# Kernel tuning notes

Measured on AMD Instinct MI355X. Metric: run time of the kernel, lower is better.

The kernel has to match this reference:

```python
import jax, jax.numpy as jnp
import numpy as np

N = 13627
E = 504378
D = 500


def _seg_softmax(e, seg, n):
    m = jax.ops.segment_max(e, seg, num_segments=n)
    ex = jnp.exp(e - m[seg])
    s = jax.ops.segment_sum(ex, seg, num_segments=n)
    return ex / (s[seg] + 1e-16)


def _gatv2(x, src, dst, Wl, Wr, att, b, n):
    # PyG GATv2Conv (heads=1): message = Wl x_src; score uses Wl x_src + Wr x_dst
    xl = x @ Wl                                   # [N, F]
    xr = x @ Wr                                   # [N, F]
    e = jax.nn.leaky_relu(xl[src] + xr[dst], 0.2) @ att   # [E]
    a = _seg_softmax(e, dst, n)                   # segment softmax over targets
    out = jax.ops.segment_sum(a[:, None] * xl[src], dst, num_segments=n)
    return out + b


def setup_inputs() -> dict:
    key = jax.random.key(0)
    ks = jax.random.split(key, 24)
    s = 0.05
    inp = {
        'x': jax.random.normal(ks[0], (N, D), dtype=jnp.float32),
        'edge_index': jax.random.randint(ks[1], (2, E), 0, N),
        'neg_edge_index': jax.random.randint(ks[2], (2, E), 0, N),
        'Wl1': jax.random.normal(ks[3], (D, 300)) * s,
        'Wr1': jax.random.normal(ks[4], (D, 300)) * s,
        'att1': jax.random.normal(ks[5], (300,)) * s,
        'b1': jnp.zeros((300,)),
        'Wl2': jax.random.normal(ks[6], (300, 100)) * s,
        'Wr2': jax.random.normal(ks[7], (300, 100)) * s,
        'att2': jax.random.normal(ks[8], (100,)) * s,
        'b2': jnp.zeros((100,)),
        'Wl3': jax.random.normal(ks[9], (100, 1)) * s,
        'Wr3': jax.random.normal(ks[10], (100, 1)) * s,
        'att3': jax.random.normal(ks[11], (1,)) * s,
        'b3': jnp.zeros((1,)),
        'W_lin1': jax.random.normal(ks[12], (D, 100)) * s,
        'b_lin1': jnp.zeros((100,)),
        'W_lin2': jax.random.normal(ks[13], (D, 100)) * s,
        'b_lin2': jnp.zeros((100,)),
        'c1': jnp.array([0.5], dtype=jnp.float32),
        'c2': jnp.array([0.5], dtype=jnp.float32),
    }
    return inp


def reference(x, edge_index, neg_edge_index, Wl1, Wr1, att1, b1, Wl2, Wr2, att2, b2,
              Wl3, Wr3, att3, b3, W_lin1, b_lin1, W_lin2, b_lin2, c1, c2):
    # eval mode: dropout / dropout_adj are identity
    loops = jnp.arange(N)
    src = jnp.concatenate([edge_index[0], loops])   # GATv2Conv adds self loops
    dst = jnp.concatenate([edge_index[1], loops])

    h1 = jax.nn.relu(_gatv2(x, src, dst, Wl1, Wr1, att1, b1, N))
    h2 = jax.nn.relu(_gatv2(h1, src, dst, Wl2, Wr2, att2, b2, N))

    xo = h2 + jax.nn.relu(x @ W_lin1 + b_lin1)
    z = h2 + jax.nn.relu(x @ W_lin2 + b_lin2)

    # link-prediction reconstruction loss
    pos_s = jnp.sum(z[edge_index[0]] * z[edge_index[1]], axis=1)
    pos_loss = -jnp.mean(jnp.log(jax.nn.sigmoid(pos_s) + 1e-15))
    neg_s = jnp.sum(z[neg_edge_index[0]] * z[neg_edge_index[1]], axis=1)
    neg_loss = -jnp.mean(jnp.log(1.0 - jax.nn.sigmoid(neg_s) + 1e-15))
    r_loss = pos_loss + neg_loss

    out = _gatv2(xo, src, dst, Wl3, Wr3, att3, b3, N)   # [N, 1]
    return out, r_loss, c1, c2
```

## Files before the change

kernel.cpp:

```cpp
#include <hip/hip_runtime.h>
#include <hip/hip_bf16.h>

#define NODES 13627
#define DIM   500

typedef short short8 __attribute__((ext_vector_type(8)));
typedef float f32x4 __attribute__((ext_vector_type(4)));
typedef float floatx2 __attribute__((ext_vector_type(2)));

__device__ inline float wave_reduce_sum(float v) {
#pragma unroll
    for (int o = 32; o > 0; o >>= 1) v += __shfl_xor(v, o, 64);
    return v;
}

__device__ inline void store_v(float* p, float v) { *p = v; }
__device__ inline void store_v(__hip_bfloat16* p, float v) { *p = __float2bfloat16(v); }

__device__ inline float blo(unsigned w) { unsigned t = w << 16;        return __builtin_bit_cast(float, t); }
__device__ inline float bhi(unsigned w) { unsigned t = w & 0xffff0000u; return __builtin_bit_cast(float, t); }

__device__ inline unsigned char to_fp8(float v) {
    int r = __builtin_amdgcn_cvt_pk_fp8_f32(v, v, 0, false);
    return (unsigned char)(r & 0xff);
}

__device__ inline unsigned pk2bf(float a, float b) {
    unsigned la = (unsigned)__builtin_bit_cast(unsigned short, __float2bfloat16(a));
    unsigned hb = (unsigned)__builtin_bit_cast(unsigned short, __float2bfloat16(b));
    return la | (hb << 16);
}

struct b4 { __hip_bfloat16 a, b, c, d; };

__global__ __launch_bounds__(256) void hist_kernel(const int* __restrict__ dst,
                                                   int* __restrict__ cnt, int E) {
    int i = blockIdx.x * blockDim.x + threadIdx.x;
    if (i < E) atomicAdd(&cnt[dst[i]], 1);
}

__global__ __launch_bounds__(1024) void scan_kernel(int* __restrict__ cnt_cur,
                                                    int* __restrict__ off, int n) {
    __shared__ int wsum[16];
    const int tid = threadIdx.x, lane = tid & 63, w = tid >> 6;
    int carry = 0;
    for (int base = 0; base < n; base += 1024) {
        int i = base + tid;
        int v = (i < n) ? cnt_cur[i] : 0;
        int s = v;
#pragma unroll
        for (int o = 1; o < 64; o <<= 1) {
            int t = __shfl_up(s, o, 64);
            if (lane >= o) s += t;
        }
        if (lane == 63) wsum[w] = s;
        __syncthreads();
        if (w == 0 && lane < 16) {
            int x = wsum[lane];
            int sx = x;
#pragma unroll
            for (int o = 1; o < 16; o <<= 1) {
                int t = __shfl_up(sx, o, 64);
                if (lane >= o) sx += t;
            }
            wsum[lane] = sx;
        }
        __syncthreads();
        int wo = (w == 0) ? 0 : wsum[w - 1];
        int total = wsum[15];
        int excl = carry + wo + (s - v);
        if (i < n) { off[i] = excl; cnt_cur[i] = excl; }
        carry += total;
        __syncthreads();
    }
    if (tid == 0) off[n] = carry;
}

__global__ __launch_bounds__(256) void scatter_kernel(const int* __restrict__ src,
                                                      const int* __restrict__ dst,
                                                      int* __restrict__ cur,
                                                      int* __restrict__ ssrc, int E) {
    int i = blockIdx.x * blockDim.x + threadIdx.x;
    if (i < E) {
        int p = atomicAdd(&cur[dst[i]], 1);
        ssrc[p] = src[i];
    }
}

__global__ __launch_bounds__(256) void convert_all_kernel(
    const float* __restrict__ x,
    const float* __restrict__ Wl1, const float* __restrict__ Wr1,
    const float* __restrict__ Wl2, const float* __restrict__ Wr2,
    const float* __restrict__ Ws1, const float* __restrict__ Ws2,
    const float* __restrict__ bs1, const float* __restrict__ bs2,
    __hip_bfloat16* __restrict__ W1T, __hip_bfloat16* __restrict__ W2T,
    __hip_bfloat16* __restrict__ WsT, float* __restrict__ bcat,
    __hip_bfloat16* __restrict__ xb, int M) {
    int i = blockIdx.x * 256 + threadIdx.x;
    if (i < 327680) {
        int n = i >> 9, k = i & 511;
        float v = 0.f;
        if (k < 500) {
            if (n < 300) v = Wl1[k * 300 + n];
            else if (n < 600) v = Wr1[k * 300 + n - 300];
        }
        W1T[i] = __float2bfloat16(v);
    } else if (i < 409600) {
        int j = i - 327680;
        int n = j / 320, k = j - n * 320;
        float v = 0.f;
        if (k < 300) {
            if (n < 100) v = Wl2[k * 100 + n];
            else if (n < 200) v = Wr2[k * 100 + n - 100];
        }
        W2T[j] = __float2bfloat16(v);
    } else if (i < 540672) {
        int j = i - 409600;
        int n = j >> 9, k = j & 511;
        float v = 0.f;
        if (k < 500) {
            if (n < 100) v = Ws1[k * 100 + n];
            else if (n < 200) v = Ws2[k * 100 + n - 100];
        }
        WsT[j] = __float2bfloat16(v);
    } else if (i < 540928) {
        int n = i - 540672;
        float v = 0.f;
        if (n < 100) v = bs1[n];
        else if (n < 200) v = bs2[n - 100];
        bcat[n] = v;
    } else {
        int j = i - 540928;
        if (j >= M * 128) return;
        int m = j >> 7, k = (j & 127) << 2;
        b4 o;
        if (k < 500) {
            float4 v = *(const float4*)(x + (size_t)m * 500 + k);
            o.a = __float2bfloat16(v.x); o.b = __float2bfloat16(v.y);
            o.c = __float2bfloat16(v.z); o.d = __float2bfloat16(v.w);
        } else {
            o.a = o.b = o.c = o.d = __float2bfloat16(0.f);
        }
        *(b4*)(xb + (size_t)m * 512 + k) = o;
    }
}

template <int EPI, typename TC>
__global__ __launch_bounds__(256) void mfma_gemm(
    const __hip_bfloat16* __restrict__ A, const __hip_bfloat16* __restrict__ BT,
    TC* __restrict__ C, const float* __restrict__ bias, const float* __restrict__ h2,
    unsigned char* __restrict__ p8, __hip_bfloat16* __restrict__ pb,
    int M, int Kp, int Nn, int ldc) {
    __shared__ short AsF[8 * 64 * 8];
    __shared__ short BsF[4 * 64 * 8];
    const int t = threadIdx.x;
    const int w = t >> 6, lane = t & 63;
    const int c = t & 3, rr = t >> 2;
    const int m0 = blockIdx.y * 128, n0 = blockIdx.x * 64;

    f32x4 acc[2][4];
#pragma unroll
    for (int i = 0; i < 2; i++)
#pragma unroll
        for (int j = 0; j < 4; j++) acc[i][j] = (f32x4){0.f, 0.f, 0.f, 0.f};

    for (int k0 = 0; k0 < Kp; k0 += 32) {
#pragma unroll
        for (int r = 0; r < 2; r++) {
            int m = r * 64 + rr;
            int gm = m0 + m; if (gm >= M) gm = M - 1;
            float4 v = *(const float4*)(A + (size_t)gm * Kp + k0 + c * 8);
            int mi = m >> 4, sl = m & 15;
            *(float4*)(&AsF[(mi * 64 + c * 16 + sl) * 8]) = v;
        }
        {
            int n = rr;
            float4 v = *(const float4*)(BT + (size_t)(n0 + n) * Kp + k0 + c * 8);
            int ni = n >> 4, sl = n & 15;
            *(float4*)(&BsF[(ni * 64 + c * 16 + sl) * 8]) = v;
        }
        __syncthreads();
        short8 a0 = *(const short8*)(&AsF[((w * 2 + 0) * 64 + lane) * 8]);
        short8 a1 = *(const short8*)(&AsF[((w * 2 + 1) * 64 + lane) * 8]);
#pragma unroll
        for (int j = 0; j < 4; j++) {
            short8 b = *(const short8*)(&BsF[(j * 64 + lane) * 8]);
            acc[0][j] = __builtin_amdgcn_mfma_f32_16x16x32_bf16(a0, b, acc[0][j], 0, 0, 0);
            acc[1][j] = __builtin_amdgcn_mfma_f32_16x16x32_bf16(a1, b, acc[1][j], 0, 0, 0);
        }
        __syncthreads();
    }

    const int q = lane >> 4, sl = lane & 15;
#pragma unroll
    for (int i = 0; i < 2; i++) {
#pragma unroll
        for (int j = 0; j < 4; j++) {
#pragma unroll
            for (int reg = 0; reg < 4; reg++) {
                int gm = m0 + w * 32 + i * 16 + q * 4 + reg;
                int gn = n0 + j * 16 + sl;
                if (gm >= M) continue;
                float v = acc[i][j][reg];
                if constexpr (EPI == 1) {
                    if (gn < 300)       p8[(size_t)gm * 304 + gn] = to_fp8(v);
                    else if (gn < 600)  pb[(size_t)gm * 320 + (gn - 300)] = __float2bfloat16(v);
                    else if (gn < 620)  pb[(size_t)gm * 320 + (gn - 300)] = __float2bfloat16(0.f);
                    else if (gn < 624)  p8[(size_t)gm * 304 + (gn - 320)] = 0;
                } else if constexpr (EPI == 2) {
                    if (gn < 100)       p8[(size_t)gm * 112 + gn] = to_fp8(v);
                    else if (gn < 200)  pb[(size_t)gm * 128 + (gn - 100)] = __float2bfloat16(v);
                    else if (gn < 212)  p8[(size_t)gm * 112 + (gn - 100)] = 0;
                    else if (gn < 240)  pb[(size_t)gm * 128 + (gn - 112)] = __float2bfloat16(0.f);
                } else if constexpr (EPI == 3) {
                    if (gn < 200) {
                        int cn = gn < 100 ? gn : gn - 100;
                        float val = fmaxf(v + bias[gn], 0.f) + h2[(size_t)gm * 100 + cn];
                        if (gn < 100) C[(size_t)gm * 100 + gn] = val;
                        else p8[(size_t)gm * 128 + (gn - 100)] = to_fp8(val);
                    } else if (gn < 228) {
                        p8[(size_t)gm * 128 + (gn - 100)] = 0;
                    }
                } else {
                    store_v(&C[(size_t)gm * ldc + gn], v);
                }
            }
        }
    }
}

template <int F, int NJ, int SL8, int SRB, int SOUT, int JSL, typename TOUT>
__global__ __launch_bounds__(256) void gat_f8_kernel(
    const unsigned char* __restrict__ xl8, const __hip_bfloat16* __restrict__ xrb,
    const float* __restrict__ att, const float* __restrict__ bias,
    const int* __restrict__ off, const int* __restrict__ ssrc,
    TOUT* __restrict__ out, int n) {
    __shared__ float sden[2];
    __shared__ float sacc[2][NJ * 64];
    const int t = threadIdx.x;
    const int lane = t & 63;
    const int sl = lane & 15, q = lane >> 4;
    const int half = (t >> 6) & 1;
    const int pairIdx = t >> 7;
    int wid = blockIdx.x * 2 + pairIdx;
    if (wid >= n) wid = n - 1;

    floatx2 attv[NJ * 2], xrv[NJ * 2], acc[NJ * 2];
    const unsigned* xru = (const unsigned*)xrb + (size_t)wid * (SRB / 2);
#pragma unroll
    for (int j = 0; j < NJ; j++) {
        const int f0 = sl * 4 + j * 64;
        if (f0 < F) {
            float4 a4 = *(const float4*)(att + f0);
            attv[j * 2 + 0] = (floatx2){a4.x, a4.y};
            attv[j * 2 + 1] = (floatx2){a4.z, a4.w};
        } else {
            attv[j * 2 + 0] = (floatx2){0.f, 0.f};
            attv[j * 2 + 1] = (floatx2){0.f, 0.f};
        }
        unsigned u0 = __builtin_nontemporal_load(xru + (f0 >> 1));
        unsigned u1 = __builtin_nontemporal_load(xru + (f0 >> 1) + 1);
        xrv[j * 2 + 0] = (floatx2){blo(u0), bhi(u0)};
        xrv[j * 2 + 1] = (floatx2){blo(u1), bhi(u1)};
        acc[j * 2 + 0] = (floatx2){0.f, 0.f};
        acc[j * 2 + 1] = (floatx2){0.f, 0.f};
    }

    const int s0 = off[wid], s1 = off[wid + 1];
    const int h0 = (s1 - s0) >> 1;
    const int eb = half ? (s0 + h0) : (s0 - 1);
    const int ee = half ? s1 : (s0 + h0);
    float den = 0.f;

    unsigned u[NJ];
    {
        int eq = eb + q;
        int src = wid;
        if (eq >= s0 && eq < ee) src = __builtin_nontemporal_load(ssrc + eq);
        const unsigned char* row = xl8 + (size_t)src * SL8;
#pragma unroll
        for (int j = 0; j < NJ; j++) {
            const bool ld = (j < NJ - 1) || (sl < JSL);
            u[j] = ld ? *(const unsigned*)(row + sl * 4 + j * 64) : 0u;
        }
    }

    for (int e0 = eb; e0 < ee; e0 += 4) {
        const bool act = (e0 + q) < ee;
        unsigned un[NJ];
        {
            int eq1 = e0 + 4 + q;
            int src1 = wid;
            if (eq1 >= s0 && eq1 < ee) src1 = __builtin_nontemporal_load(ssrc + eq1);
            const unsigned char* row1 = xl8 + (size_t)src1 * SL8;
#pragma unroll
            for (int j = 0; j < NJ; j++) {
                const bool ld = (j < NJ - 1) || (sl < JSL);
                un[j] = ld ? *(const unsigned*)(row1 + sl * 4 + j * 64) : 0u;
            }
        }
        floatx2 xlv[NJ * 2];
        floatx2 p2 = (floatx2){0.f, 0.f};
#pragma unroll
        for (int j = 0; j < NJ; j++) {
            floatx2 lo = __builtin_amdgcn_cvt_pk_f32_fp8((int)u[j], false);
            floatx2 hi = __builtin_amdgcn_cvt_pk_f32_fp8((int)u[j], true);
            xlv[j * 2 + 0] = lo;
            xlv[j * 2 + 1] = hi;
            floatx2 s0v = lo + xrv[j * 2 + 0];
            floatx2 s1v = hi + xrv[j * 2 + 1];
            floatx2 g0 = __builtin_elementwise_max(s0v, 0.2f * s0v);
            floatx2 g1 = __builtin_elementwise_max(s1v, 0.2f * s1v);
            p2 += attv[j * 2 + 0] * g0;
            p2 += attv[j * 2 + 1] * g1;
        }
        float p = p2.x + p2.y;
        p += __shfl_xor(p, 1, 64);
        p += __shfl_xor(p, 2, 64);
        p += __shfl_xor(p, 4, 64);
        p += __shfl_xor(p, 8, 64);
        float ex = act ? expf(p) : 0.f;
        den += ex;
        floatx2 ex2 = (floatx2){ex, ex};
#pragma unroll
        for (int i = 0; i < NJ * 2; i++) acc[i] += ex2 * xlv[i];
#pragma unroll
        for (int j = 0; j < NJ; j++) u[j] = un[j];
    }

    float* af = (float*)acc;
#pragma unroll
    for (int o = 16; o <= 32; o <<= 1) {
        den += __shfl_xor(den, o, 64);
#pragma unroll
        for (int i = 0; i < NJ * 4; i++) af[i] += __shfl_xor(af[i], o, 64);
    }

    if (half == 1 && lane < 16) {
        if (lane == 0) sden[pairIdx] = den;
#pragma unroll
        for (int j = 0; j < NJ; j++)
            *(float4*)(&sacc[pairIdx][sl * 4 + j * 64]) =
                make_float4(af[j * 4 + 0], af[j * 4 + 1], af[j * 4 + 2], af[j * 4 + 3]);
    }
    __syncthreads();
    if (half == 0 && lane < 16) {
        den += sden[pairIdx];
        const float inv = 1.f / (den + 1e-16f);
#pragma unroll
        for (int j = 0; j < NJ; j++) {
            const int f0 = sl * 4 + j * 64;
            if (f0 >= SOUT) continue;
            float4 o4 = *(float4*)(&sacc[pairIdx][f0]);
            float vv[4] = {af[j * 4 + 0] + o4.x, af[j * 4 + 1] + o4.y,
                           af[j * 4 + 2] + o4.z, af[j * 4 + 3] + o4.w};
            float r[4];
#pragma unroll
            for (int cc = 0; cc < 4; cc++) {
                const int f = f0 + cc;
                float v = 0.f;
                if (f < F) v = fmaxf(vv[cc] * inv + bias[f], 0.f);
                r[cc] = v;
            }
            if constexpr (sizeof(TOUT) == 4) {
                *(float4*)((float*)out + (size_t)wid * SOUT + f0) =
                    make_float4(r[0], r[1], r[2], r[3]);
            } else {
                unsigned* op = (unsigned*)out + (size_t)wid * (SOUT / 2) + (f0 >> 1);
                op[0] = pk2bf(r[0], r[1]);
                op[1] = pk2bf(r[2], r[3]);
            }
        }
    }
}

__global__ __launch_bounds__(256) void gemm_vec1_kernel(
    const float* __restrict__ xo, const float* __restrict__ wl,
    const float* __restrict__ wr, float* __restrict__ xl3,
    float* __restrict__ xr3, int M, int ldx) {
    const int wid = blockIdx.x * 4 + (threadIdx.x >> 6);
    const int lane = threadIdx.x & 63;
    if (wid >= M) return;
    float a = 0.f, b = 0.f;
    for (int f = lane; f < 100; f += 64) {
        float v = xo[(size_t)wid * ldx + f];
        a += v * wl[f];
        b += v * wr[f];
    }
    a = wave_reduce_sum(a);
    b = wave_reduce_sum(b);
    if (lane == 0) { xl3[wid] = a; xr3[wid] = b; }
}

__global__ __launch_bounds__(256) void gat3_kernel(
    const float* __restrict__ xl3, const float* __restrict__ xr3,
    const float* __restrict__ att3, const float* __restrict__ b3,
    const int* __restrict__ off, const int* __restrict__ ssrc,
    float* __restrict__ out, int n) {
    const int wid = blockIdx.x * 4 + (threadIdx.x >> 6);
    const int lane = threadIdx.x & 63;
    if (wid >= n) return;
    const float xrv = xr3[wid];
    const float att = att3[0];
    float num = 0.f, den = 0.f;
    const int s0 = off[wid], s1 = off[wid + 1];
    for (int e = s0 - 1 + lane; e < s1; e += 64) {
        int src = (e < s0) ? wid : ssrc[e];
        float xlv = xl3[src];
        float t = xlv + xrv;
        float g = t > 0.f ? t : 0.2f * t;
        float ex = expf(g * att);
        den += ex;
        num += ex * xlv;
    }
    num = wave_reduce_sum(num);
    den = wave_reduce_sum(den);
    if (lane == 0) out[wid] = num / (den + 1e-16f) + b3[0];
}

__global__ __launch_bounds__(256) void loss_kernel(
    const unsigned char* __restrict__ z8, const int* __restrict__ pos,
    const int* __restrict__ neg, float* __restrict__ part, int nb, int E) {
    const int lane = threadIdx.x & 63;
    const int sl = lane & 15;
    const int wlocal = threadIdx.x >> 6;
    const int q = lane >> 4;
    const int nq = gridDim.x * 16;
    const int qid = (blockIdx.x * 4 + wlocal) * 4 + q;
    const int total = 2 * E;
    float psum = 0.f, nsum = 0.f;

    for (int base = qid; base < total; base += 4 * nq) {
        uint2 au[4], bu[4];
        bool act[4], isN[4];
#pragma unroll
        for (int s = 0; s < 4; s++) {
            int it = base + s * nq;
            act[s] = it < total;
            int itc = act[s] ? it : 0;
            isN[s] = itc >= E;
            int e = isN[s] ? itc - E : itc;
            const int* ei = isN[s] ? neg : pos;
            int u = ei[e], v = ei[E + e];
            au[s] = *(const uint2*)(z8 + (size_t)u * 128 + sl * 8);
            bu[s] = *(const uint2*)(z8 + (size_t)v * 128 + sl * 8);
        }
#pragma unroll
        for (int s = 0; s < 4; s++) {
            floatx2 a0 = __builtin_amdgcn_cvt_pk_f32_fp8((int)au[s].x, false);
            floatx2 a1 = __builtin_amdgcn_cvt_pk_f32_fp8((int)au[s].x, true);
            floatx2 a2 = __builtin_amdgcn_cvt_pk_f32_fp8((int)au[s].y, false);
            floatx2 a3 = __builtin_amdgcn_cvt_pk_f32_fp8((int)au[s].y, true);
            floatx2 b0 = __builtin_amdgcn_cvt_pk_f32_fp8((int)bu[s].x, false);
            floatx2 b1 = __builtin_amdgcn_cvt_pk_f32_fp8((int)bu[s].x, true);
            floatx2 b2 = __builtin_amdgcn_cvt_pk_f32_fp8((int)bu[s].y, false);
            floatx2 b3 = __builtin_amdgcn_cvt_pk_f32_fp8((int)bu[s].y, true);
            float p = a0.x * b0.x + a0.y * b0.y + a1.x * b1.x + a1.y * b1.y
                    + a2.x * b2.x + a2.y * b2.y + a3.x * b3.x + a3.y * b3.y;
            p += __shfl_xor(p, 1, 64);
            p += __shfl_xor(p, 2, 64);
            p += __shfl_xor(p, 4, 64);
            p += __shfl_xor(p, 8, 64);
            if (sl == 0 && act[s]) {
                float sig = 1.f / (1.f + expf(-p));
                if (isN[s]) nsum += logf(1.f - sig + 1e-15f);
                else        psum += logf(sig + 1e-15f);
            }
        }
    }
    float pw = wave_reduce_sum(psum);
    float nw = wave_reduce_sum(nsum);
    __shared__ float sp[4], sn[4];
    if (lane == 0) { sp[wlocal] = pw; sn[wlocal] = nw; }
    __syncthreads();
    if (threadIdx.x == 0) {
        part[blockIdx.x]      = sp[0] + sp[1] + sp[2] + sp[3];
        part[nb + blockIdx.x] = sn[0] + sn[1] + sn[2] + sn[3];
    }
}

__global__ __launch_bounds__(1024) void finalize_kernel(
    const float* __restrict__ part, int nb,
    const float* __restrict__ c1, const float* __restrict__ c2,
    float* __restrict__ out, int n, int E) {
    __shared__ float sp[16], sn[16];
    const int tid = threadIdx.x, lane = tid & 63, w = tid >> 6;
    float p = 0.f, q = 0.f;
    for (int i = tid; i < nb; i += 1024) { p += part[i]; q += part[nb + i]; }
    p = wave_reduce_sum(p);
    q = wave_reduce_sum(q);
    if (lane == 0) { sp[w] = p; sn[w] = q; }
    __syncthreads();
    if (tid == 0) {
        float tp = 0.f, tq = 0.f;
#pragma unroll
        for (int i = 0; i < 16; i++) { tp += sp[i]; tq += sn[i]; }
        out[n]     = -(tp + tq) / (float)E;
        out[n + 1] = c1[0];
        out[n + 2] = c2[0];
    }
}

extern "C" void kernel_launch(void* const* d_in, const int* in_sizes, int n_in,
                              void* d_out, int out_size, void* d_ws, size_t ws_size,
                              hipStream_t stream) {
    const float* x      = (const float*)d_in[0];
    const int*   ei     = (const int*)d_in[1];
    const int*   nei    = (const int*)d_in[2];
    const float* Wl1    = (const float*)d_in[3];
    const float* Wr1    = (const float*)d_in[4];
    const float* att1   = (const float*)d_in[5];
    const float* b1     = (const float*)d_in[6];
    const float* Wl2    = (const float*)d_in[7];
    const float* Wr2    = (const float*)d_in[8];
    const float* att2   = (const float*)d_in[9];
    const float* b2     = (const float*)d_in[10];
    const float* Wl3    = (const float*)d_in[11];
    const float* Wr3    = (const float*)d_in[12];
    const float* att3   = (const float*)d_in[13];
    const float* b3     = (const float*)d_in[14];
    const float* Wlin1  = (const float*)d_in[15];
    const float* blin1  = (const float*)d_in[16];
    const float* Wlin2  = (const float*)d_in[17];
    const float* blin2  = (const float*)d_in[18];
    const float* c1     = (const float*)d_in[19];
    const float* c2     = (const float*)d_in[20];
    float* out = (float*)d_out;

    const int E = in_sizes[1] / 2;
    const int N = NODES;
    const int LOSS_BLOCKS = 4096;

    char* ws = (char*)d_ws;
    unsigned char*  xl8  = (unsigned char*)(ws + 0);
    unsigned char*  xl28 = (unsigned char*)(ws + 0);
    __hip_bfloat16* xrb  = (__hip_bfloat16*)(ws + 4194304);
    __hip_bfloat16* xr2b = (__hip_bfloat16*)(ws + 4194304);
    float*          xo   = (float*)(ws + 4194304);
    unsigned char*  z8   = (unsigned char*)(ws + 9645312);
    __hip_bfloat16* h1b  = (__hip_bfloat16*)(ws + 12915712);
    float*          h2   = (float*)(ws + 12915712);
    __hip_bfloat16* xb   = (__hip_bfloat16*)(ws + 21637120);
    __hip_bfloat16* W1T  = (__hip_bfloat16*)(ws + 35591168);
    __hip_bfloat16* W2T  = (__hip_bfloat16*)(ws + 36246528);
    __hip_bfloat16* WsT  = (__hip_bfloat16*)(ws + 36410368);
    float*          bcat = (float*)(ws + 36672512);
    float*          xl3  = (float*)(ws + 36673536);
    float*          xr3  = (float*)(ws + 36728064);
    int*            ioff = (int*)(ws + 36782592);
    int*            cur  = (int*)(ws + 36837376);
    int*            ssrc = (int*)(ws + 36892160);
    float*          part = (float*)(ws + 38909952);

    hipMemsetAsync(cur, 0, sizeof(int) * N, stream);

    hist_kernel<<<(E + 255) / 256, 256, 0, stream>>>(ei + E, cur, E);
    scan_kernel<<<1, 1024, 0, stream>>>(cur, ioff, N);
    scatter_kernel<<<(E + 255) / 256, 256, 0, stream>>>(ei, ei + E, cur, ssrc, E);

    convert_all_kernel<<<(540928 + N * 128 + 255) / 256, 256, 0, stream>>>(
        x, Wl1, Wr1, Wl2, Wr2, Wlin1, Wlin2, blin1, blin2,
        W1T, W2T, WsT, bcat, xb, N);

    mfma_gemm<1, __hip_bfloat16><<<dim3(10, 107), 256, 0, stream>>>(
        xb, W1T, (__hip_bfloat16*)nullptr, nullptr, nullptr, xl8, xrb, N, 512, 640, 0);
    gat_f8_kernel<300, 5, 304, 320, 320, 11, __hip_bfloat16>
        <<<(N + 1) / 2, 256, 0, stream>>>(xl8, xrb, att1, b1, ioff, ssrc, h1b, N);

    mfma_gemm<2, __hip_bfloat16><<<dim3(4, 107), 256, 0, stream>>>(
        h1b, W2T, (__hip_bfloat16*)nullptr, nullptr, nullptr, xl28, xr2b, N, 320, 256, 0);
    gat_f8_kernel<100, 2, 112, 128, 100, 9, float>
        <<<(N + 1) / 2, 256, 0, stream>>>(xl28, xr2b, att2, b2, ioff, ssrc, h2, N);

    mfma_gemm<3, float><<<dim3(4, 107), 256, 0, stream>>>(
        xb, WsT, xo, bcat, h2, z8, nullptr, N, 512, 256, 0);

    loss_kernel<<<LOSS_BLOCKS, 256, 0, stream>>>(z8, ei, nei, part, LOSS_BLOCKS, E);

    gemm_vec1_kernel<<<(N + 3) / 4, 256, 0, stream>>>(xo, Wl3, Wr3, xl3, xr3, N, 100);
    gat3_kernel<<<(N + 3) / 4, 256, 0, stream>>>(xl3, xr3, att3, b3, ioff, ssrc, out, N);

    finalize_kernel<<<1, 1024, 0, stream>>>(part, LOSS_BLOCKS, c1, c2, out, N, E);
}
```

Measured before the change: 387.7 us.

## Assign one wavefront per GAT node and prefetch edge sources two steps ahead

The GAT aggregation kernel previously split each destination node's edge list across two wavefronts and combined their partial sums through shared memory with a block barrier. Now each wavefront processes one whole node (four nodes per block), which removes the shared-memory combine and the __syncthreads. The source-index load is also pipelined one extra iteration ahead so the index is ready before the feature-row gather. The trade-off is less parallelism per node, so a high-degree node takes longer within its wave, and the extra prefetched index adds register pressure.

```diff
diff --git a/kernel.cpp b/kernel.cpp
--- a/kernel.cpp
+++ b/kernel.cpp
@@ -235,14 +235,10 @@
     const float* __restrict__ att, const float* __restrict__ bias,
     const int* __restrict__ off, const int* __restrict__ ssrc,
     TOUT* __restrict__ out, int n) {
-    __shared__ float sden[2];
-    __shared__ float sacc[2][NJ * 64];
     const int t = threadIdx.x;
     const int lane = t & 63;
     const int sl = lane & 15, q = lane >> 4;
-    const int half = (t >> 6) & 1;
-    const int pairIdx = t >> 7;
-    int wid = blockIdx.x * 2 + pairIdx;
+    int wid = blockIdx.x * 4 + (t >> 6);
     if (wid >= n) wid = n - 1;
 
     floatx2 attv[NJ * 2], xrv[NJ * 2], acc[NJ * 2];
@@ -267,36 +263,42 @@
     }
 
     const int s0 = off[wid], s1 = off[wid + 1];
-    const int h0 = (s1 - s0) >> 1;
-    const int eb = half ? (s0 + h0) : (s0 - 1);
-    const int ee = half ? s1 : (s0 + h0);
+    const int eb = s0 - 1;
+    const int ee = s1;
     float den = 0.f;
-
+    const int myoff = sl * 4;
+
+    int srcB;
     unsigned u[NJ];
     {
-        int eq = eb + q;
-        int src = wid;
-        if (eq >= s0 && eq < ee) src = __builtin_nontemporal_load(ssrc + eq);
-        const unsigned char* row = xl8 + (size_t)src * SL8;
+        int eq0 = eb + q;
+        int srcA = wid;
+        if (eq0 >= s0 && eq0 < ee) srcA = __builtin_nontemporal_load(ssrc + eq0);
+        int eq1 = eb + 4 + q;
+        srcB = wid;
+        if (eq1 >= s0 && eq1 < ee) srcB = __builtin_nontemporal_load(ssrc + eq1);
+        const unsigned char* row = xl8 + (size_t)srcA * SL8;
 #pragma unroll
         for (int j = 0; j < NJ; j++) {
             const bool ld = (j < NJ - 1) || (sl < JSL);
-            u[j] = ld ? *(const unsigned*)(row + sl * 4 + j * 64) : 0u;
+            u[j] = ld ? *(const unsigned*)(row + myoff + j * 64) : 0u;
         }
     }
 
     for (int e0 = eb; e0 < ee; e0 += 4) {
         const bool act = (e0 + q) < ee;
+        int srcC = wid;
+        {
+            int eq2 = e0 + 8 + q;
+            if (eq2 >= s0 && eq2 < ee) srcC = __builtin_nontemporal_load(ssrc + eq2);
+        }
         unsigned un[NJ];
         {
-            int eq1 = e0 + 4 + q;
-            int src1 = wid;
-            if (eq1 >= s0 && eq1 < ee) src1 = __builtin_nontemporal_load(ssrc + eq1);
-            const unsigned char* row1 = xl8 + (size_t)src1 * SL8;
+            const unsigned char* row1 = xl8 + (size_t)srcB * SL8;
 #pragma unroll
             for (int j = 0; j < NJ; j++) {
                 const bool ld = (j < NJ - 1) || (sl < JSL);
-                un[j] = ld ? *(const unsigned*)(row1 + sl * 4 + j * 64) : 0u;
+                un[j] = ld ? *(const unsigned*)(row1 + myoff + j * 64) : 0u;
             }
         }
         floatx2 xlv[NJ * 2];
@@ -326,6 +328,7 @@
         for (int i = 0; i < NJ * 2; i++) acc[i] += ex2 * xlv[i];
 #pragma unroll
         for (int j = 0; j < NJ; j++) u[j] = un[j];
+        srcB = srcC;
     }
 
     float* af = (float*)acc;
@@ -336,30 +339,18 @@
         for (int i = 0; i < NJ * 4; i++) af[i] += __shfl_xor(af[i], o, 64);
     }
 
-    if (half == 1 && lane < 16) {
-        if (lane == 0) sden[pairIdx] = den;
-#pragma unroll
-        for (int j = 0; j < NJ; j++)
-            *(float4*)(&sacc[pairIdx][sl * 4 + j * 64]) =
-                make_float4(af[j * 4 + 0], af[j * 4 + 1], af[j * 4 + 2], af[j * 4 + 3]);
-    }
-    __syncthreads();
-    if (half == 0 && lane < 16) {
-        den += sden[pairIdx];
+    if (q == 0) {
         const float inv = 1.f / (den + 1e-16f);
 #pragma unroll
         for (int j = 0; j < NJ; j++) {
             const int f0 = sl * 4 + j * 64;
             if (f0 >= SOUT) continue;
-            float4 o4 = *(float4*)(&sacc[pairIdx][f0]);
-            float vv[4] = {af[j * 4 + 0] + o4.x, af[j * 4 + 1] + o4.y,
-                           af[j * 4 + 2] + o4.z, af[j * 4 + 3] + o4.w};
             float r[4];
 #pragma unroll
             for (int cc = 0; cc < 4; cc++) {
                 const int f = f0 + cc;
                 float v = 0.f;
-                if (f < F) v = fmaxf(vv[cc] * inv + bias[f], 0.f);
+                if (f < F) v = fmaxf(af[j * 4 + cc] * inv + bias[f], 0.f);
                 r[cc] = v;
             }
             if constexpr (sizeof(TOUT) == 4) {
@@ -565,12 +556,12 @@
     mfma_gemm<1, __hip_bfloat16><<<dim3(10, 107), 256, 0, stream>>>(
         xb, W1T, (__hip_bfloat16*)nullptr, nullptr, nullptr, xl8, xrb, N, 512, 640, 0);
     gat_f8_kernel<300, 5, 304, 320, 320, 11, __hip_bfloat16>
-        <<<(N + 1) / 2, 256, 0, stream>>>(xl8, xrb, att1, b1, ioff, ssrc, h1b, N);
+        <<<(N + 3) / 4, 256, 0, stream>>>(xl8, xrb, att1, b1, ioff, ssrc, h1b, N);
 
     mfma_gemm<2, __hip_bfloat16><<<dim3(4, 107), 256, 0, stream>>>(
         h1b, W2T, (__hip_bfloat16*)nullptr, nullptr, nullptr, xl28, xr2b, N, 320, 256, 0);
     gat_f8_kernel<100, 2, 112, 128, 100, 9, float>
-        <<<(N + 1) / 2, 256, 0, stream>>>(xl28, xr2b, att2, b2, ioff, ssrc, h2, N);
+        <<<(N + 3) / 4, 256, 0, stream>>>(xl28, xr2b, att2, b2, ioff, ssrc, h2, N);
 
     mfma_gemm<3, float><<<dim3(4, 107), 256, 0, stream>>>(
         xb, WsT, xo, bcat, h2, z8, nullptr, N, 512, 256, 0);
```

Result: faster. 376.7 us (-2.8%).
